# Kernel optimization log

Measured on AMD Instinct MI355X. Metric: run time of the kernel, lower is better.

Reference implementation:

```python
import jax, jax.numpy as jnp
import numpy as np

B, H, W, C = 8, 64, 64, 256
NUM_GROUPS = 32
EPS = 1e-6  # flax GroupNorm default


def setup_inputs() -> dict:
    key = jax.random.key(0)
    ks = jax.random.split(key, 9)
    x = jax.random.normal(ks[0], (B, H, W, C), dtype=jnp.float32)
    init = lambda k, shape: jax.random.normal(k, shape, dtype=jnp.float32) * 0.02
    return {
        "x": x,
        "gn_scale": jnp.ones((C,), jnp.float32),
        "gn_bias": jnp.zeros((C,), jnp.float32),
        "wq": init(ks[1], (C, C)), "bq": jnp.zeros((C,), jnp.float32),
        "wk": init(ks[2], (C, C)), "bk": jnp.zeros((C,), jnp.float32),
        "wv": init(ks[3], (C, C)), "bv": jnp.zeros((C,), jnp.float32),
        "wo": init(ks[4], (C, C)), "bo": jnp.zeros((C,), jnp.float32),
    }


def group_norm(x, scale, bias, num_groups, eps):
    b, h, w, c = x.shape
    xg = x.reshape(b, h, w, num_groups, c // num_groups)
    mean = jnp.mean(xg, axis=(1, 2, 4), keepdims=True)
    var = jnp.mean(jnp.square(xg - mean), axis=(1, 2, 4), keepdims=True)
    xn = (xg - mean) * jax.lax.rsqrt(var + eps)
    return xn.reshape(b, h, w, c) * scale + bias


def reference(x, gn_scale, gn_bias, wq, bq, wk, bk, wv, bv, wo, bo):
    b, h, w, c = x.shape
    hn = group_norm(x, gn_scale, gn_bias, NUM_GROUPS, EPS)
    hf = hn.reshape(b, h * w, c)  # (B, S, C)
    q = hf @ wq + bq
    k = hf @ wk + bk
    v = hf @ wv + bv
    scaling = jnp.sqrt(jnp.float32(c)).astype(x.dtype)
    attn = jax.nn.softmax(jnp.einsum('bsc,btc->bst', q, k) / scaling, axis=-1)
    out = jnp.einsum('bst,btc->bsc', attn, v)
    out = out @ wo + bo
    return out.reshape(b, h, w, c) + x
```

## Files before the change

kernel.cpp:

```cpp
#include <hip/hip_runtime.h>

#define NB   8
#define SS   4096
#define CC   256
#define NG   32
#define CPG  8
#define EPSV 1e-6f
#define MTOT (NB * SS)

typedef short bf16x8 __attribute__((ext_vector_type(8)));
typedef unsigned short u16x8 __attribute__((ext_vector_type(8)));
typedef float f32x4  __attribute__((ext_vector_type(4)));
typedef float f32x16 __attribute__((ext_vector_type(16)));
typedef int   i32x4  __attribute__((ext_vector_type(4)));
typedef int   i32x8  __attribute__((ext_vector_type(8)));
typedef unsigned char u8;

typedef __attribute__((address_space(1))) const unsigned int as1_u32;
typedef __attribute__((address_space(3))) unsigned int as3_u32;

__device__ __forceinline__ unsigned short f2bf(float f) {
  unsigned int u = __builtin_bit_cast(unsigned int, f);
  u = (u + 0x7FFFu + ((u >> 16) & 1u)) >> 16;
  return (unsigned short)u;
}
__device__ __forceinline__ u8 f2fp8(float f) {
  return (u8)(__builtin_amdgcn_cvt_pk_fp8_f32(f, f, 0, 0) & 0xFF);
}
__device__ __forceinline__ void dma16(const u8* src, u8* lds) {
  __builtin_amdgcn_global_load_lds((as1_u32*)src, (as3_u32*)lds, 16, 0, 0);
}
__device__ __forceinline__ float fast_exp2(float x) {
#if __has_builtin(__builtin_amdgcn_exp2f)
  return __builtin_amdgcn_exp2f(x);
#else
  return exp2f(x);
#endif
}

__global__ __launch_bounds__(256) void gn_stats_part_kernel(
    const float* __restrict__ x, float* __restrict__ part) {
  const int b = blockIdx.x >> 5, slice = blockIdx.x & 31;
  const int tid = threadIdx.x;
  const int g = tid & 31;
  const int p8 = tid >> 5;
  const float* base = x + ((size_t)(b * SS + slice * 128 + p8) * CC + g * CPG);
  float s = 0.f, ss = 0.f;
#pragma unroll
  for (int it = 0; it < 16; it++) {
    const float4* p = (const float4*)(base + (size_t)it * 8 * CC);
    float4 a = p[0], c = p[1];
    s  += (a.x + a.y) + (a.z + a.w) + (c.x + c.y) + (c.z + c.w);
    ss += (a.x*a.x + a.y*a.y) + (a.z*a.z + a.w*a.w)
        + (c.x*c.x + c.y*c.y) + (c.z*c.z + c.w*c.w);
  }
  s  += __shfl_xor(s, 32);
  ss += __shfl_xor(ss, 32);
  __shared__ float lsum[4][32], lssum[4][32];
  const int wv = tid >> 6, lane = tid & 63;
  if (lane < 32) { lsum[wv][lane] = s; lssum[wv][lane] = ss; }
  __syncthreads();
  if (tid < 32) {
    float ts  = (lsum[0][tid] + lsum[1][tid]) + (lsum[2][tid] + lsum[3][tid]);
    float tss = (lssum[0][tid] + lssum[1][tid]) + (lssum[2][tid] + lssum[3][tid]);
    float* dst = part + ((size_t)(b * 32 + tid) * 32 + slice) * 2;
    dst[0] = ts; dst[1] = tss;
  }
}

__global__ __launch_bounds__(256) void prep_wt_kernel(
    const float* __restrict__ w0, const float* __restrict__ w1,
    const float* __restrict__ w2, const float* __restrict__ w3,
    unsigned short* __restrict__ wt,
    const float* __restrict__ part, float* __restrict__ stats) {
  __shared__ float t[64][68];
  if (blockIdx.y == 4) {
    if (blockIdx.x == 0) {
      const int bg = threadIdx.x;
      const float* src = part + (size_t)bg * 64;
      float s = 0.f, ss = 0.f;
#pragma unroll
      for (int sl = 0; sl < 32; sl++) { s += src[sl * 2]; ss += src[sl * 2 + 1]; }
      const float inv = 1.f / (float)(SS * CPG);
      float mean = s * inv;
      float var  = ss * inv - mean * mean;
      stats[bg * 2]     = mean;
      stats[bg * 2 + 1] = rsqrtf(var + EPSV);
    }
    return;
  }
  int which = blockIdx.y;
  const float* W = (which == 0) ? w0 : (which == 1) ? w1 : (which == 2) ? w2 : w3;
  int tx = (blockIdx.x & 3) * 64;
  int ty = (blockIdx.x >> 2) * 64;
  int tid = threadIdx.x;
  int row = tid >> 4;
  int col = (tid & 15) * 4;
#pragma unroll
  for (int i = 0; i < 4; i++) {
    float4 v = *(const float4*)(W + (size_t)(ty + row + i * 16) * CC + tx + col);
    *(float4*)(&t[row + i * 16][col]) = v;
  }
  __syncthreads();
#pragma unroll
  for (int i = 0; i < 4; i++) {
    int n = row + i * 16;
    ushort4 o;
    o.x = f2bf(t[col + 0][n]);
    o.y = f2bf(t[col + 1][n]);
    o.z = f2bf(t[col + 2][n]);
    o.w = f2bf(t[col + 3][n]);
    *(ushort4*)(wt + (size_t)which * CC * CC + (size_t)(tx + n) * CC + ty + col) = o;
  }
}

__global__ __launch_bounds__(256) void gn_norm_kernel(const float* __restrict__ x,
                                                      const float* __restrict__ stats,
                                                      const float* __restrict__ gamma,
                                                      const float* __restrict__ beta,
                                                      unsigned short* __restrict__ hn) {
  int i8 = blockIdx.x * 256 + threadIdx.x;
  int c8 = (i8 & 31) * 8;
  size_t row = (size_t)(i8 >> 5);
  int b = (int)(row >> 12);
  int sidx = (b * NG + (c8 >> 3)) * 2;
  float mean = stats[sidx], rstd = stats[sidx + 1];
  const float4* xp = (const float4*)(x + row * CC + c8);
  float4 v0 = xp[0], v1 = xp[1];
  const float4* gp = (const float4*)(gamma + c8);
  float4 g0 = gp[0], g1 = gp[1];
  const float4* bp = (const float4*)(beta + c8);
  float4 b0 = bp[0], b1 = bp[1];
  u16x8 o;
  o[0] = f2bf((v0.x - mean) * rstd * g0.x + b0.x);
  o[1] = f2bf((v0.y - mean) * rstd * g0.y + b0.y);
  o[2] = f2bf((v0.z - mean) * rstd * g0.z + b0.z);
  o[3] = f2bf((v0.w - mean) * rstd * g0.w + b0.w);
  o[4] = f2bf((v1.x - mean) * rstd * g1.x + b1.x);
  o[5] = f2bf((v1.y - mean) * rstd * g1.y + b1.y);
  o[6] = f2bf((v1.z - mean) * rstd * g1.z + b1.z);
  o[7] = f2bf((v1.w - mean) * rstd * g1.w + b1.w);
  *(u16x8*)(hn + row * CC + c8) = o;
}


__global__ __launch_bounds__(256) void qkv_gemm_kernel(
    const unsigned short* __restrict__ A,
    const unsigned short* __restrict__ WT,
    const float* __restrict__ bq, const float* __restrict__ bk, const float* __restrict__ bv,
    u8* __restrict__ qo, u8* __restrict__ ko, u8* __restrict__ vt) {
  __shared__ __align__(1024) u8 smem[65536];
  u8* As0 = smem;
  u8* As1 = smem + 16384;
  u8* Bs  = smem + 32768;

  const int which = blockIdx.z;
  const u8* Bwb = (const u8*)(WT + (size_t)which * CC * CC);
  const float* bias = (which == 0) ? bq : (which == 1) ? bk : bv;

  const int m0 = blockIdx.x * 256;
  const int n0 = blockIdx.y * 64;
  const int tid = threadIdx.x;
  const int wave = tid >> 6, lane = tid & 63;
  const int l32 = lane & 31, h = lane >> 5;

  const u8* Ab = (const u8*)A;

  const int am = tid >> 2;
  const int aslot = tid & 3;
  const size_t asrc_row = (size_t)(m0 + am) * 512;
  const int asrc_ch = ((aslot ^ (am & 3)) << 4);
  const int bn = tid >> 5;
  const int bslot = tid & 31;

#pragma unroll
  for (int i = 0; i < 8; i++) {
    int n = i * 8 + bn;
    dma16(Bwb + (size_t)(n0 + n) * 512 + ((bslot ^ (n & 31)) << 4),
          Bs + i * 4096 + tid * 16);
  }
#pragma unroll
  for (int i = 0; i < 4; i++)
    dma16(Ab + asrc_row + (size_t)i * 64 * 512 + asrc_ch, As0 + i * 4096 + tid * 16);
  __syncthreads();

  f32x16 acc[2][2] = {};
  const int arow0 = (wave * 64 + l32) * 64;
  const int nrow0 = l32 * 512;
  const int aswz = l32 & 3;
  const int bswz = l32;

#pragma unroll
  for (int s = 0; s < 8; ++s) {
    u8* cur = (s & 1) ? As1 : As0;
    if (s < 7) {
      u8* nxt = (s & 1) ? As0 : As1;
      size_t koff = (size_t)(s + 1) * 64;
#pragma unroll
      for (int i = 0; i < 4; i++)
        dma16(Ab + asrc_row + (size_t)i * 64 * 512 + koff + asrc_ch,
              nxt + i * 4096 + tid * 16);
    }
#pragma unroll
    for (int ks = 0; ks < 2; ks++) {
      bf16x8 af0 = *(const bf16x8*)(cur + arow0 + (((h + 2 * ks) ^ aswz) << 4));
      bf16x8 af1 = *(const bf16x8*)(cur + arow0 + 32 * 64 + (((h + 2 * ks) ^ aswz) << 4));
      bf16x8 bf0 = *(const bf16x8*)(Bs + nrow0 + (((s * 4 + h + 2 * ks) ^ bswz) << 4));
      bf16x8 bf1 = *(const bf16x8*)(Bs + nrow0 + 32 * 512 + (((s * 4 + h + 2 * ks) ^ bswz) << 4));
      acc[0][0] = __builtin_amdgcn_mfma_f32_32x32x16_bf16(af0, bf0, acc[0][0], 0, 0, 0);
      acc[0][1] = __builtin_amdgcn_mfma_f32_32x32x16_bf16(af0, bf1, acc[0][1], 0, 0, 0);
      acc[1][0] = __builtin_amdgcn_mfma_f32_32x32x16_bf16(af1, bf0, acc[1][0], 0, 0, 0);
      acc[1][1] = __builtin_amdgcn_mfma_f32_32x32x16_bf16(af1, bf1, acc[1][1], 0, 0, 0);
    }
    __syncthreads();
  }

  if (which < 2) {
    u8* out = (which == 0) ? qo : ko;
#pragma unroll
    for (int nt = 0; nt < 2; nt++) {
      int n = n0 + nt * 32 + l32;
      float bv_ = bias[n];
#pragma unroll
      for (int mt = 0; mt < 2; mt++)
#pragma unroll
        for (int r = 0; r < 16; r++) {
          int m = m0 + wave * 64 + mt * 32 + (r & 3) + 8 * (r >> 2) + 4 * h;
          out[(size_t)m * CC + n] = f2fp8(acc[mt][nt][r] + bv_);
        }
    }
  } else {
    int bb = m0 >> 12;
#pragma unroll
    for (int nt = 0; nt < 2; nt++) {
      int n = n0 + nt * 32 + l32;
      float bv_ = bias[n];
#pragma unroll
      for (int mt = 0; mt < 2; mt++)
#pragma unroll
        for (int g = 0; g < 4; g++) {
          int mg = m0 + wave * 64 + mt * 32 + g * 8 + 4 * h;
          int w = __builtin_amdgcn_cvt_pk_fp8_f32(acc[mt][nt][g*4+0] + bv_, acc[mt][nt][g*4+1] + bv_, 0, 0);
          w = __builtin_amdgcn_cvt_pk_fp8_f32(acc[mt][nt][g*4+2] + bv_, acc[mt][nt][g*4+3] + bv_, w, 1);
          *(unsigned int*)(vt + (size_t)bb * CC * SS + (size_t)n * SS + (mg & 4095)) = (unsigned int)w;
        }
    }
  }
}

__global__ __launch_bounds__(256) void out_gemm_kernel(
    const unsigned short* __restrict__ A,
    const unsigned short* __restrict__ WT,
    const float* __restrict__ bias,
    const float* __restrict__ residual,
    float* __restrict__ Of) {
  __shared__ __align__(1024) u8 smem[65536];
  u8* As0 = smem;
  u8* As1 = smem + 16384;
  u8* Bs  = smem + 32768;

  const u8* Bwb = (const u8*)(WT + (size_t)3 * CC * CC);
  const int m0 = blockIdx.x * 256;
  const int n0 = blockIdx.y * 64;
  const int tid = threadIdx.x;
  const int wave = tid >> 6, lane = tid & 63;
  const int l32 = lane & 31, h = lane >> 5;

  const u8* Ab = (const u8*)A;
  const int am = tid >> 2;
  const int aslot = tid & 3;
  const size_t asrc_row = (size_t)(m0 + am) * 512;
  const int asrc_ch = ((aslot ^ (am & 3)) << 4);
  const int bn = tid >> 5;
  const int bslot = tid & 31;

#pragma unroll
  for (int i = 0; i < 8; i++) {
    int n = i * 8 + bn;
    dma16(Bwb + (size_t)(n0 + n) * 512 + ((bslot ^ (n & 31)) << 4),
          Bs + i * 4096 + tid * 16);
  }
#pragma unroll
  for (int i = 0; i < 4; i++)
    dma16(Ab + asrc_row + (size_t)i * 64 * 512 + asrc_ch, As0 + i * 4096 + tid * 16);
  __syncthreads();

  f32x16 acc[2][2] = {};
  const int arow0 = (wave * 64 + l32) * 64;
  const int nrow0 = l32 * 512;
  const int aswz = l32 & 3;
  const int bswz = l32;

#pragma unroll
  for (int s = 0; s < 8; ++s) {
    u8* cur = (s & 1) ? As1 : As0;
    if (s < 7) {
      u8* nxt = (s & 1) ? As0 : As1;
      size_t koff = (size_t)(s + 1) * 64;
#pragma unroll
      for (int i = 0; i < 4; i++)
        dma16(Ab + asrc_row + (size_t)i * 64 * 512 + koff + asrc_ch,
              nxt + i * 4096 + tid * 16);
    }
#pragma unroll
    for (int ks = 0; ks < 2; ks++) {
      bf16x8 af0 = *(const bf16x8*)(cur + arow0 + (((h + 2 * ks) ^ aswz) << 4));
      bf16x8 af1 = *(const bf16x8*)(cur + arow0 + 32 * 64 + (((h + 2 * ks) ^ aswz) << 4));
      bf16x8 bf0 = *(const bf16x8*)(Bs + nrow0 + (((s * 4 + h + 2 * ks) ^ bswz) << 4));
      bf16x8 bf1 = *(const bf16x8*)(Bs + nrow0 + 32 * 512 + (((s * 4 + h + 2 * ks) ^ bswz) << 4));
      acc[0][0] = __builtin_amdgcn_mfma_f32_32x32x16_bf16(af0, bf0, acc[0][0], 0, 0, 0);
      acc[0][1] = __builtin_amdgcn_mfma_f32_32x32x16_bf16(af0, bf1, acc[0][1], 0, 0, 0);
      acc[1][0] = __builtin_amdgcn_mfma_f32_32x32x16_bf16(af1, bf0, acc[1][0], 0, 0, 0);
      acc[1][1] = __builtin_amdgcn_mfma_f32_32x32x16_bf16(af1, bf1, acc[1][1], 0, 0, 0);
    }
    __syncthreads();
  }

#pragma unroll
  for (int nt = 0; nt < 2; nt++) {
    int n = n0 + nt * 32 + l32;
    float bv_ = bias[n];
#pragma unroll
    for (int mt = 0; mt < 2; mt++)
#pragma unroll
      for (int r = 0; r < 16; r++) {
        int m = m0 + wave * 64 + mt * 32 + (r & 3) + 8 * (r >> 2) + 4 * h;
        Of[(size_t)m * CC + n] = acc[mt][nt][r] + bv_ + residual[(size_t)m * CC + n];
      }
  }
}

#define BR 64

__global__ __launch_bounds__(256, 3) void flash_attn_kernel(
    const u8* __restrict__ Qg,
    const u8* __restrict__ Kg,
    const u8* __restrict__ Vtg,
    unsigned short* __restrict__ Og) {
  __shared__ __align__(1024) u8 smem[53760];
  u8* KB0 = smem;
  u8* KB1 = smem + 16384;
  u8* VB  = smem + 32768;
  u8* Ps  = smem + 49152;
  float* Lred = (float*)(smem + 53248);

  const int bid = blockIdx.x;
  const int b = bid & 7, q0 = (bid >> 3) * BR;
  const int tid = threadIdx.x;
  const int wave = tid >> 6, lane = tid & 63;
  const int l32 = lane & 31, h = lane >> 5;
  const int wm = wave >> 1, wc = wave & 1;

  const u8* Qb  = Qg  + (size_t)b * SS * CC;
  const u8* Kb  = Kg  + (size_t)b * SS * CC;
  const u8* Vtb = Vtg + (size_t)b * CC * SS;

  const int kkey = tid >> 4, kc16 = tid & 15;
  const u8* ksrc0 = Kb + (size_t)kkey * CC + ((kc16 ^ (kkey & 15)) << 4);
  const int vch = tid >> 2;
  const int vs  = (tid & 3) ^ (vch & 3);
  const u8* vsrc0 = Vtb + (size_t)vch * SS + (vs << 4);

  i32x8 qf[4];
  {
    const u8* qrow = Qb + (size_t)(q0 + wm * 32 + l32) * CC + h * 32;
#pragma unroll
    for (int t = 0; t < 4; t++) qf[t] = *(const i32x8*)(qrow + t * 64);
  }

  f32x16 oacc[4] = {};
  float ll = 0.f;

#pragma unroll
  for (int i = 0; i < 4; i++)
    dma16(ksrc0 + (size_t)i * 16 * CC, KB0 + i * 4096 + tid * 16);

  const int kswz = l32 & 15;
  const int vswz = l32 & 3;
  const int pswz = l32 & 7;

  for (int j = 0; j < SS / BR; ++j) {
    const u8* Kcur = (j & 1) ? KB1 : KB0;
    u8* Knxt = (j & 1) ? KB0 : KB1;

    __syncthreads();
    {
      size_t vbase = (size_t)j * 64;
#pragma unroll
      for (int i = 0; i < 4; i++)
        dma16(vsrc0 + (size_t)i * 64 * SS + vbase, VB + i * 4096 + tid * 16);
    }

    {
      f32x16 sacc = {};
      const u8* kb = Kcur + (wc * 32 + l32) * 256;
      __builtin_amdgcn_s_setprio(1);
#pragma unroll
      for (int t = 0; t < 4; t++) {
        i32x4 r0 = *(const i32x4*)(kb + (((t * 4 + 2 * h)     ^ kswz) << 4));
        i32x4 r1 = *(const i32x4*)(kb + (((t * 4 + 2 * h + 1) ^ kswz) << 4));
        i32x8 kf = __builtin_shufflevector(r0, r1, 0, 1, 2, 3, 4, 5, 6, 7);
        sacc = __builtin_amdgcn_mfma_scale_f32_32x32x64_f8f6f4(
            kf, qf[t], sacc, 0, 0, 0, 0x7F7F7F7F, 0, 0x7F7F7F7F);
      }
      __builtin_amdgcn_s_setprio(0);
      u8* pb = Ps + (wm * 32 + l32) * 64;
#pragma unroll
      for (int g = 0; g < 4; g++) {
        float p0 = fast_exp2(fminf(sacc[g * 4 + 0] * 0.09016844f, 7.213475f));
        float p1 = fast_exp2(fminf(sacc[g * 4 + 1] * 0.09016844f, 7.213475f));
        float p2 = fast_exp2(fminf(sacc[g * 4 + 2] * 0.09016844f, 7.213475f));
        float p3 = fast_exp2(fminf(sacc[g * 4 + 3] * 0.09016844f, 7.213475f));
        ll += (p0 + p1) + (p2 + p3);
        int wv_ = __builtin_amdgcn_cvt_pk_fp8_f32(p0, p1, 0, 0);
        wv_ = __builtin_amdgcn_cvt_pk_fp8_f32(p2, p3, wv_, 1);
        *(unsigned int*)(pb + (((wc * 4 + g) ^ pswz) << 3) + 4 * h) = (unsigned int)wv_;
      }
    }

    __syncthreads();
    if (j + 1 < SS / BR) {
      size_t krow = (size_t)(j + 1) * 64;
#pragma unroll
      for (int i = 0; i < 4; i++)
        dma16(ksrc0 + (krow + (size_t)i * 16) * CC, Knxt + i * 4096 + tid * 16);
    }

    {
      unsigned long pf[4];
      const u8* pb = Ps + (wm * 32 + l32) * 64;
#pragma unroll
      for (int ki = 0; ki < 4; ki++)
        pf[ki] = *(const unsigned long*)(pb + (((4 * h + ki) ^ pswz) << 3));
      i32x8 pa;
#pragma unroll
      for (int ki = 0; ki < 4; ki++) {
        pa[2 * ki]     = (int)(unsigned int)pf[ki];
        pa[2 * ki + 1] = (int)(unsigned int)(pf[ki] >> 32);
      }
      __builtin_amdgcn_s_setprio(1);
#pragma unroll
      for (int nt = 0; nt < 4; nt++) {
        const u8* vb = VB + (wc * 128 + nt * 32 + l32) * 64;
        i32x4 r0 = *(const i32x4*)(vb + (((2 * h)     ^ vswz) << 4));
        i32x4 r1 = *(const i32x4*)(vb + (((2 * h + 1) ^ vswz) << 4));
        i32x8 vf = __builtin_shufflevector(r0, r1, 0, 1, 2, 3, 4, 5, 6, 7);
        oacc[nt] = __builtin_amdgcn_mfma_scale_f32_32x32x64_f8f6f4(
            pa, vf, oacc[nt], 0, 0, 0, 0x7F7F7F7F, 0, 0x7F7F7F7F);
      }
      __builtin_amdgcn_s_setprio(0);
    }
  }

  ll += __shfl_xor(ll, 32);
  if (h == 0) Lred[wc * 64 + wm * 32 + l32] = ll;
  __syncthreads();

#pragma unroll
  for (int r = 0; r < 16; r++) {
    int row = (r & 3) + 8 * (r >> 2) + 4 * h;
    float inv = 1.f / (Lred[wm * 32 + row] + Lred[64 + wm * 32 + row]);
    size_t base = ((size_t)b * SS + q0 + wm * 32 + row) * CC + wc * 128 + l32;
#pragma unroll
    for (int nt = 0; nt < 4; nt++)
      Og[base + nt * 32] = f2bf(oacc[nt][r] * inv);
  }
}

extern "C" void kernel_launch(void* const* d_in, const int* in_sizes, int n_in,
                              void* d_out, int out_size, void* d_ws, size_t ws_size,
                              hipStream_t stream) {
  const float* x   = (const float*)d_in[0];
  const float* gsc = (const float*)d_in[1];
  const float* gbi = (const float*)d_in[2];
  const float* wq  = (const float*)d_in[3];
  const float* bq  = (const float*)d_in[4];
  const float* wk  = (const float*)d_in[5];
  const float* bk  = (const float*)d_in[6];
  const float* wv  = (const float*)d_in[7];
  const float* bv  = (const float*)d_in[8];
  const float* wo  = (const float*)d_in[9];
  const float* bo  = (const float*)d_in[10];
  float* out = (float*)d_out;

  char* ws = (char*)d_ws;
  const size_t MAT = (size_t)MTOT * CC;
  float* stats        = (float*)ws;
  unsigned short* wt  = (unsigned short*)(ws + 4096);
  unsigned short* hn  = wt + (size_t)4 * CC * CC;
  unsigned short* ao  = hn + MAT;
  u8* q  = (u8*)(ao + MAT);
  u8* k  = q + MAT;
  u8* vt = k + MAT;

  float* part = (float*)ao;

  gn_stats_part_kernel<<<NB * NG, 256, 0, stream>>>(x, part);
  prep_wt_kernel<<<dim3(16, 5), 256, 0, stream>>>(wq, wk, wv, wo, wt, part, stats);
  gn_norm_kernel<<<(int)(MAT / 8 / 256), 256, 0, stream>>>(x, stats, gsc, gbi, hn);

  qkv_gemm_kernel<<<dim3(MTOT / 256, CC / 64, 3), 256, 0, stream>>>(
      hn, wt, bq, bk, bv, q, k, vt);

  flash_attn_kernel<<<NB * (SS / BR), 256, 0, stream>>>(q, k, vt, ao);

  out_gemm_kernel<<<dim3(MTOT / 256, CC / 64), 256, 0, stream>>>(ao, wt, bo, x, out);
}
```

Baseline: 245.8 us.

## Split attention over two KV halves and add a combine kernel

```diff
diff --git a/kernel.cpp b/kernel.cpp
--- a/kernel.cpp
+++ b/kernel.cpp
@@ -336,16 +336,17 @@
     const u8* __restrict__ Qg,
     const u8* __restrict__ Kg,
     const u8* __restrict__ Vtg,
-    unsigned short* __restrict__ Og) {
-  __shared__ __align__(1024) u8 smem[53760];
-  u8* KB0 = smem;
-  u8* KB1 = smem + 16384;
-  u8* VB  = smem + 32768;
-  u8* Ps  = smem + 49152;
-  float* Lred = (float*)(smem + 53248);
+    unsigned short* __restrict__ po0,
+    unsigned short* __restrict__ po1,
+    float* __restrict__ pl) {
+  __shared__ __align__(1024) u8 smem[41984];
+  u8* KB = smem;
+  u8* VB = smem + 16384;
+  u8* Ps = smem + 32768;
+  float* Lred = (float*)(smem + 41472);
 
   const int bid = blockIdx.x;
-  const int b = bid & 7, q0 = (bid >> 3) * BR;
+  const int b = bid & 7, q0 = ((bid >> 3) & 63) * BR, ks = bid >> 9;
   const int tid = threadIdx.x;
   const int wave = tid >> 6, lane = tid & 63;
   const int l32 = lane & 31, h = lane >> 5;
@@ -371,17 +372,18 @@
   f32x16 oacc[4] = {};
   float ll = 0.f;
 
+  const int j0 = ks * 32;
+
 #pragma unroll
   for (int i = 0; i < 4; i++)
-    dma16(ksrc0 + (size_t)i * 16 * CC, KB0 + i * 4096 + tid * 16);
+    dma16(ksrc0 + ((size_t)j0 * 64 + (size_t)i * 16) * CC, KB + i * 4096 + tid * 16);
 
   const int kswz = l32 & 15;
   const int vswz = l32 & 3;
   const int pswz = l32 & 7;
 
-  for (int j = 0; j < SS / BR; ++j) {
-    const u8* Kcur = (j & 1) ? KB1 : KB0;
-    u8* Knxt = (j & 1) ? KB0 : KB1;
+  for (int jt = 0; jt < 32; ++jt) {
+    const int j = j0 + jt;
 
     __syncthreads();
     {
@@ -393,7 +395,7 @@
 
     {
       f32x16 sacc = {};
-      const u8* kb = Kcur + (wc * 32 + l32) * 256;
+      const u8* kb = KB + (wc * 32 + l32) * 256;
       __builtin_amdgcn_s_setprio(1);
 #pragma unroll
       for (int t = 0; t < 4; t++) {
@@ -404,7 +406,7 @@
             kf, qf[t], sacc, 0, 0, 0, 0x7F7F7F7F, 0, 0x7F7F7F7F);
       }
       __builtin_amdgcn_s_setprio(0);
-      u8* pb = Ps + (wm * 32 + l32) * 64;
+      u8* pb = Ps + (wm * 32 + l32) * 136;
 #pragma unroll
       for (int g = 0; g < 4; g++) {
         float p0 = fast_exp2(fminf(sacc[g * 4 + 0] * 0.09016844f, 7.213475f));
@@ -419,16 +421,16 @@
     }
 
     __syncthreads();
-    if (j + 1 < SS / BR) {
+    if (jt + 1 < 32) {
       size_t krow = (size_t)(j + 1) * 64;
 #pragma unroll
       for (int i = 0; i < 4; i++)
-        dma16(ksrc0 + (krow + (size_t)i * 16) * CC, Knxt + i * 4096 + tid * 16);
+        dma16(ksrc0 + (krow + (size_t)i * 16) * CC, KB + i * 4096 + tid * 16);
     }
 
     {
       unsigned long pf[4];
-      const u8* pb = Ps + (wm * 32 + l32) * 64;
+      const u8* pb = Ps + (wm * 32 + l32) * 136;
 #pragma unroll
       for (int ki = 0; ki < 4; ki++)
         pf[ki] = *(const unsigned long*)(pb + (((4 * h + ki) ^ pswz) << 3));
@@ -456,15 +458,36 @@
   if (h == 0) Lred[wc * 64 + wm * 32 + l32] = ll;
   __syncthreads();
 
+  unsigned short* po = (ks == 0) ? po0 : po1;
+  if (tid < 64)
+    pl[(size_t)ks * MTOT + (size_t)b * SS + q0 + tid] = Lred[tid] + Lred[64 + tid];
+
 #pragma unroll
   for (int r = 0; r < 16; r++) {
     int row = (r & 3) + 8 * (r >> 2) + 4 * h;
-    float inv = 1.f / (Lred[wm * 32 + row] + Lred[64 + wm * 32 + row]);
     size_t base = ((size_t)b * SS + q0 + wm * 32 + row) * CC + wc * 128 + l32;
 #pragma unroll
     for (int nt = 0; nt < 4; nt++)
-      Og[base + nt * 32] = f2bf(oacc[nt][r] * inv);
-  }
+      po[base + nt * 32] = f2bf(oacc[nt][r]);
+  }
+}
+
+__global__ __launch_bounds__(256) void combine_kernel(
+    const unsigned short* __restrict__ po0, const unsigned short* __restrict__ po1,
+    const float* __restrict__ pl, unsigned short* __restrict__ ao) {
+  int i8 = blockIdx.x * 256 + threadIdx.x;
+  size_t row = (size_t)(i8 >> 5);
+  float inv = 1.f / (pl[row] + pl[(size_t)MTOT + row]);
+  u16x8 a  = *(const u16x8*)(po0 + (size_t)i8 * 8);
+  u16x8 c  = *(const u16x8*)(po1 + (size_t)i8 * 8);
+  u16x8 o;
+#pragma unroll
+  for (int t = 0; t < 8; t++) {
+    float fa = __builtin_bit_cast(float, (unsigned int)a[t] << 16);
+    float fc = __builtin_bit_cast(float, (unsigned int)c[t] << 16);
+    o[t] = f2bf((fa + fc) * inv);
+  }
+  *(u16x8*)(ao + (size_t)i8 * 8) = o;
 }
 
 extern "C" void kernel_launch(void* const* d_in, const int* in_sizes, int n_in,
@@ -492,6 +515,7 @@
   u8* q  = (u8*)(ao + MAT);
   u8* k  = q + MAT;
   u8* vt = k + MAT;
+  float* pl = (float*)(vt + MAT);
 
   float* part = (float*)ao;
 
@@ -502,7 +526,9 @@
   qkv_gemm_kernel<<<dim3(MTOT / 256, CC / 64, 3), 256, 0, stream>>>(
       hn, wt, bq, bk, bv, q, k, vt);
 
-  flash_attn_kernel<<<NB * (SS / BR), 256, 0, stream>>>(q, k, vt, ao);
+  flash_attn_kernel<<<NB * (SS / BR) * 2, 256, 0, stream>>>(q, k, vt, ao, hn, pl);
+
+  combine_kernel<<<(int)(MAT / 8 / 256), 256, 0, stream>>>(ao, hn, pl, ao);
 
   out_gemm_kernel<<<dim3(MTOT / 256, CC / 64), 256, 0, stream>>>(ao, wt, bo, x, out);
 }
```

Result: slower. 258.5 us (+5.2%).
